# Kernel optimization log

Hardware: AMD Instinct MI355X
Metric: run time of the kernel (lower is better)

## Reference

```python
import jax, jax.numpy as jnp
import numpy as np

N_EMBD = 1024
HEAD_SIZE = 64

def setup_inputs() -> dict:
    key = jax.random.key(0)
    kx, kk, kq, kv = jax.random.split(key, 4)
    x = jax.random.normal(kx, (8, 2048, N_EMBD), dtype=jnp.float32)
    scale = 1.0 / np.sqrt(N_EMBD)
    # nn.Linear weights are [out, in]; kaiming-uniform-ish init
    Wk = jax.random.uniform(kk, (HEAD_SIZE, N_EMBD), dtype=jnp.float32, minval=-scale, maxval=scale)
    Wq = jax.random.uniform(kq, (HEAD_SIZE, N_EMBD), dtype=jnp.float32, minval=-scale, maxval=scale)
    Wv = jax.random.uniform(kv, (HEAD_SIZE, N_EMBD), dtype=jnp.float32, minval=-scale, maxval=scale)
    return {"x": x, "Wk": Wk, "Wq": Wq, "Wv": Wv}

def reference(x, Wk, Wq, Wv):
    # x: [B, T, E]; W*: [H, E] (torch Linear layout)
    k = jnp.einsum('bte,he->bth', x, Wk)
    q = jnp.einsum('bte,he->bth', x, Wq)
    v = jnp.einsum('bte,he->bth', x, Wv)
    inv_sqrt_h = 1.0 / np.sqrt(HEAD_SIZE)
    wei = jnp.einsum('bth,bsh->bts', q, k) * inv_sqrt_h  # [B, T, T]
    wei = jax.nn.softmax(wei, axis=-1)
    out = jnp.einsum('bts,bsh->bth', wei, v)  # [B, T, H]
    return out
```

## Files before the change

### kernel.cpp

```cpp
#include <hip/hip_runtime.h>
#include <cstdint>

#define NB 8
#define TS 2048
#define NE 1024
#define HD 64
#define MTOT (NB*TS)

typedef float     f4  __attribute__((ext_vector_type(4)));
typedef short     s8v __attribute__((ext_vector_type(8)));
typedef short     s4v __attribute__((ext_vector_type(4)));
typedef int       i4v __attribute__((ext_vector_type(4)));
typedef _Float16  h8  __attribute__((ext_vector_type(8)));

__device__ __forceinline__ short f2bf(float f) {
  union { float f; uint32_t u; } x; x.f = f;
  return (short)((x.u + 0x7FFFu + ((x.u >> 16) & 1u)) >> 16);
}

__device__ __forceinline__ int pack2(float lo, float hi) {
  union { float f; uint32_t u; } a, b; a.f = lo; b.f = hi;
  return (int)__builtin_amdgcn_perm(b.u + 0x8000u, a.u + 0x8000u, 0x07060302u);
}

__device__ __forceinline__ void gl2lds(const void* gptr, void* lptr) {
  auto g = (const __attribute__((address_space(1))) uint32_t*)gptr;
  auto l = (__attribute__((address_space(3))) uint32_t*)lptr;
  __builtin_amdgcn_global_load_lds(g, l, 16, 0, 0);
}

template <int N>
__device__ __forceinline__ void wait_barrier() {
  asm volatile("s_waitcnt vmcnt(%0) lgkmcnt(0)" :: "n"(N) : "memory");
  __builtin_amdgcn_s_barrier();
}

__global__ __launch_bounds__(256) void wconv_kernel(
    const float* __restrict__ Wk, const float* __restrict__ Wq, const float* __restrict__ Wv,
    short* __restrict__ wb)
{
  const int idx = (blockIdx.x * 256 + threadIdx.x) * 4;
  const int p = idx >> 16;
  const int off = idx & 65535;
  const float* W = (p == 0) ? Wq : (p == 1) ? Wk : Wv;
  const float s = (p == 0) ? 0.18033688011112042f : 1.0f;
  const float4 v = *(const float4*)&W[off];
  s4v h; h[0] = f2bf(v.x*s); h[1] = f2bf(v.y*s); h[2] = f2bf(v.z*s); h[3] = f2bf(v.w*s);
  *(s4v*)&wb[idx] = h;
}

__global__ __launch_bounds__(256) void proj_kernel(
    const float* __restrict__ x, const short* __restrict__ wb,
    short* __restrict__ qo, short* __restrict__ ko, _Float16* __restrict__ vo)
{
  __shared__ float Xs[4][32][64];
  __shared__ short Ws[2][192][64];
  const int tid = threadIdx.x;
  const int wv = tid >> 6, lane = tid & 63, n = lane & 15, quad = lane >> 4;
  const int mg = wv & 1, cg = wv >> 1;
  const int r0 = blockIdx.x * 32;
  const int xrow = lane >> 4, xslot = lane & 15;
  const int wrow = lane >> 3, wslot = lane & 7;

  auto dmaX = [&](int c, int buf) {
#pragma unroll
    for (int u = 0; u < 2; ++u) {
      const int R0 = (wv * 2 + u) * 4;
      const int row = R0 + xrow;
      const int gs = (xslot + row) & 15;
      gl2lds(&x[(size_t)(r0 + row) * NE + c * 64 + gs * 4], &Xs[buf][R0][0]);
    }
  };
  auto dmaW = [&](int c, int buf) {
#pragma unroll
    for (int u = 0; u < 6; ++u) {
      const int C0 = (wv * 6 + u) * 8;
      const int col = C0 + wrow;
      const int gs = (wslot + col) & 7;
      gl2lds(&wb[(size_t)col * NE + c * 64 + gs * 8], &Ws[buf][C0][0]);
    }
  };

  const f4 fz = {0.f, 0.f, 0.f, 0.f};
  f4 acc[6] = {fz, fz, fz, fz, fz, fz};

  auto compute = [&](int bw, int bx) {
    s8v a[2];
    const int row = mg * 16 + n;
#pragma unroll
    for (int kc = 0; kc < 2; ++kc) {
      const int u0 = kc * 8 + quad * 2;
      const float* pr = &Xs[bx][row][0];
      const f4 f0 = *(const f4*)(pr + (((u0    ) - row) & 15) * 4);
      const f4 f1 = *(const f4*)(pr + (((u0 + 1) - row) & 15) * 4);
      i4v ai;
      ai[0] = pack2(f0[0], f0[1]); ai[1] = pack2(f0[2], f0[3]);
      ai[2] = pack2(f1[0], f1[1]); ai[3] = pack2(f1[2], f1[3]);
      a[kc] = __builtin_bit_cast(s8v, ai);
    }
#pragma unroll
    for (int nf = 0; nf < 6; ++nf) {
      const int col = cg * 96 + nf * 16 + n;
      const s8v b0 = *(const s8v*)&Ws[bw][col][(((0 + quad) - col) & 7) * 8];
      const s8v b1 = *(const s8v*)&Ws[bw][col][(((4 + quad) - col) & 7) * 8];
      acc[nf] = __builtin_amdgcn_mfma_f32_16x16x32_bf16(a[0], b0, acc[nf], 0, 0, 0);
      acc[nf] = __builtin_amdgcn_mfma_f32_16x16x32_bf16(a[1], b1, acc[nf], 0, 0, 0);
    }
  };

  dmaW(0, 0); dmaX(0, 0); dmaX(1, 1); dmaX(2, 2);
  wait_barrier<4>();

  for (int t = 0; t < 16; ++t) {
    if (t <= 14) dmaW(t + 1, (t + 1) & 1);
    if (t <= 12) dmaX(t + 3, (t + 3) & 3);
    compute(t & 1, t & 3);
    if (t <= 12)      wait_barrier<2>();
    else if (t <= 14) wait_barrier<0>();
  }

#pragma unroll
  for (int nf = 0; nf < 6; ++nf) {
    const int gc = cg * 96 + nf * 16;
    const int p = gc >> 6;
    const int rcol = (gc & 63) + n;
#pragma unroll
    for (int i = 0; i < 4; ++i) {
      const int R = r0 + mg * 16 + quad * 4 + i;
      const float av = acc[nf][i];
      if (p == 0)      qo[(size_t)R * HD + rcol] = f2bf(av);
      else if (p == 1) ko[(size_t)R * HD + rcol] = f2bf(av);
      else {
        const int t2 = R & (TS - 1), b = t2 & 31;
        const int pos = (t2 & ~31) | (((b >> 2) & 3) << 3) | (((b >> 4) & 1) << 2) | (b & 3);
        vo[(size_t)(R >> 11) * HD * TS + (size_t)rcol * TS + pos] = (_Float16)av;
      }
    }
  }
}

__global__ __launch_bounds__(512) void attn_kernel(
    const short* __restrict__ q, const short* __restrict__ k,
    const _Float16* __restrict__ vT, float* __restrict__ out)
{
  __shared__ __align__(16) char smem[98304];
  const int tid = threadIdx.x;
  const int wv = tid >> 6, lane = tid & 63, n = lane & 15, quad = lane >> 4;
  const int kq = wv & 3, qg = wv >> 2;
  const int batch = blockIdx.x & 7;
  const int qgb = blockIdx.x >> 3;
  const int m0 = batch * TS + qgb * 64;
  const short*    kb = k  + (size_t)batch * TS * HD;
  const _Float16* vb = vT + (size_t)batch * HD * TS;
  const int drow = lane >> 3, dslot = lane & 7;
  const f4 fz = {0.f, 0.f, 0.f, 0.f};

  auto kbuf = [&](int buf) { return (short*)(smem + (kq * 3 + buf) * 8192); };

  auto dmaK = [&](int tt, int buf) {
    const int c = kq * 8 + tt;
#pragma unroll
    for (int u = 0; u < 4; ++u) {
      const int K0 = (qg * 4 + u) * 8;
      const int key = K0 + drow;
      const int gs = (dslot + key) & 7;
      gl2lds(&kb[(size_t)(c * 64 + key) * HD + gs * 8], kbuf(buf) + K0 * 64);
    }
  };

  s8v qf[2][2];
#pragma unroll
  for (int qh = 0; qh < 2; ++qh)
#pragma unroll
    for (int kc = 0; kc < 2; ++kc)
      qf[qh][kc] = *(const s8v*)&q[(size_t)(m0 + qg * 32 + qh * 16 + n) * HD + kc * 32 + quad * 8];

  f4 o[2][4] = {{fz, fz, fz, fz}, {fz, fz, fz, fz}};
  f4 lD[2] = {fz, fz};
  h8 ones;
#pragma unroll
  for (int j = 0; j < 8; ++j) ones[j] = (_Float16)1.0f;

  dmaK(0, 0); dmaK(1, 1);
  wait_barrier<4>();

  for (int t = 0; t < 8; ++t) {
    const int buf = t % 3;
    const int c = kq * 8 + t;

    h8 vfr[2][4];
#pragma unroll
    for (int pr = 0; pr < 2; ++pr)
#pragma unroll
      for (int g = 0; g < 4; ++g)
        vfr[pr][g] = *(const h8*)&vb[(size_t)(g * 16 + n) * TS + c * 64 + (pr * 4 + quad) * 8];

    if (t <= 5) dmaK(t + 2, (t + 2) % 3);

    const short* ks = kbuf(buf);
    s8v kf[4][2];
#pragma unroll
    for (int f = 0; f < 4; ++f)
#pragma unroll
      for (int kc = 0; kc < 2; ++kc) {
        const int key = f * 16 + n;
        kf[f][kc] = *(const s8v*)&ks[key * 64 + (((kc * 4 + quad) - key) & 7) * 8];
      }

    f4 st[2][4];
#pragma unroll
    for (int qh = 0; qh < 2; ++qh)
#pragma unroll
      for (int f = 0; f < 4; ++f) {
        st[qh][f] = __builtin_amdgcn_mfma_f32_16x16x32_bf16(kf[f][0], qf[qh][0], fz, 0, 0, 0);
        st[qh][f] = __builtin_amdgcn_mfma_f32_16x16x32_bf16(kf[f][1], qf[qh][1], st[qh][f], 0, 0, 0);
      }

    h8 pa[2][2];
#pragma unroll
    for (int qh = 0; qh < 2; ++qh)
#pragma unroll
      for (int pr = 0; pr < 2; ++pr)
#pragma unroll
        for (int hf = 0; hf < 2; ++hf)
#pragma unroll
          for (int i = 0; i < 4; ++i)
            pa[qh][pr][hf * 4 + i] = (_Float16)__builtin_amdgcn_exp2f(st[qh][pr * 2 + hf][i]);

#pragma unroll
    for (int pr = 0; pr < 2; ++pr) {
#pragma unroll
      for (int qh = 0; qh < 2; ++qh)
        lD[qh] = __builtin_amdgcn_mfma_f32_16x16x32_f16(pa[qh][pr], ones, lD[qh], 0, 0, 0);
#pragma unroll
      for (int g = 0; g < 4; ++g)
#pragma unroll
        for (int qh = 0; qh < 2; ++qh)
          o[qh][g] = __builtin_amdgcn_mfma_f32_16x16x32_f16(pa[qh][pr], vfr[pr][g], o[qh][g], 0, 0, 0);
    }

    if (t <= 5)      wait_barrier<4>();
    else if (t == 6) wait_barrier<0>();
  }

  __syncthreads();

  float* o_c = (float*)smem;
  float* l_c = (float*)(smem + 69632);
  if (n == 0)
#pragma unroll
    for (int qh = 0; qh < 2; ++qh)
#pragma unroll
      for (int i = 0; i < 4; ++i)
        l_c[kq * 64 + qg * 32 + qh * 16 + quad * 4 + i] = lD[qh][i];
#pragma unroll
  for (int qh = 0; qh < 2; ++qh)
#pragma unroll
    for (int g = 0; g < 4; ++g)
#pragma unroll
      for (int i = 0; i < 4; ++i)
        o_c[kq * 4352 + (qg * 32 + qh * 16 + quad * 4 + i) * 68 + g * 16 + n] = o[qh][g][i];
  __syncthreads();

#pragma unroll
  for (int rep = 0; rep < 2; ++rep) {
    const int idx = tid + rep * 512;
    const int qr = idx >> 4, d4 = (idx & 15) * 4;
    float L = 0.f;
    f4 r = fz;
#pragma unroll
    for (int c2 = 0; c2 < 4; ++c2) {
      L += l_c[c2 * 64 + qr];
      r += *(const f4*)&o_c[c2 * 4352 + qr * 68 + d4];
    }
    const float inv = 1.0f / L;
    r[0] *= inv; r[1] *= inv; r[2] *= inv; r[3] *= inv;
    *(f4*)&out[(size_t)(m0 + qr) * HD + d4] = r;
  }
}

extern "C" void kernel_launch(void* const* d_in, const int* in_sizes, int n_in,
                              void* d_out, int out_size, void* d_ws, size_t ws_size,
                              hipStream_t stream) {
  const float* x  = (const float*)d_in[0];
  const float* Wk = (const float*)d_in[1];
  const float* Wq = (const float*)d_in[2];
  const float* Wv = (const float*)d_in[3];
  float* out = (float*)d_out;

  short* qb = (short*)d_ws;
  short* kb = qb + (size_t)MTOT * HD;
  _Float16* vb = (_Float16*)(kb + (size_t)MTOT * HD);
  short* wb = (short*)(vb + (size_t)NB * HD * TS);

  wconv_kernel<<<192, 256, 0, stream>>>(Wk, Wq, Wv, wb);
  proj_kernel<<<MTOT / 32, 256, 0, stream>>>(x, wb, qb, kb, vb);
  attn_kernel<<<MTOT / 64, 512, 0, stream>>>(qb, kb, vb, out);
}
```

Baseline: 139.7 us.

## Stage V tiles through LDS with async DMA alongside K, double-buffered

V fragments are no longer loaded straight from global memory into registers. They are now DMA'd into LDS with the same swizzled global_load_lds path as K. The K ring goes from three buffers to two, and V gets a matching double buffer, growing shared memory to 128KB. An extra LDS-done barrier comes before each refill so a buffer is not overwritten while still being read. This trades extra barriers and larger LDS use for coalesced, asynchronous V loads and fewer scattered direct reads.

```diff
diff --git a/kernel.cpp b/kernel.cpp
--- a/kernel.cpp
+++ b/kernel.cpp
@@ -32,6 +32,11 @@
 template <int N>
 __device__ __forceinline__ void wait_barrier() {
   asm volatile("s_waitcnt vmcnt(%0) lgkmcnt(0)" :: "n"(N) : "memory");
+  __builtin_amdgcn_s_barrier();
+}
+
+__device__ __forceinline__ void lds_done_barrier() {
+  asm volatile("s_waitcnt lgkmcnt(0)" ::: "memory");
   __builtin_amdgcn_s_barrier();
 }
 
@@ -143,7 +148,7 @@
     const short* __restrict__ q, const short* __restrict__ k,
     const _Float16* __restrict__ vT, float* __restrict__ out)
 {
-  __shared__ __align__(16) char smem[98304];
+  __shared__ __align__(16) char smem[131072];
   const int tid = threadIdx.x;
   const int wv = tid >> 6, lane = tid & 63, n = lane & 15, quad = lane >> 4;
   const int kq = wv & 3, qg = wv >> 2;
@@ -155,9 +160,10 @@
   const int drow = lane >> 3, dslot = lane & 7;
   const f4 fz = {0.f, 0.f, 0.f, 0.f};
 
-  auto kbuf = [&](int buf) { return (short*)(smem + (kq * 3 + buf) * 8192); };
-
-  auto dmaK = [&](int tt, int buf) {
+  auto kbuf = [&](int buf) { return (short*)   (smem +         (kq * 2 + buf) * 8192); };
+  auto vbuf = [&](int buf) { return (_Float16*)(smem + 65536 + (kq * 2 + buf) * 8192); };
+
+  auto dmaKV = [&](int tt, int buf) {
     const int c = kq * 8 + tt;
 #pragma unroll
     for (int u = 0; u < 4; ++u) {
@@ -166,6 +172,13 @@
       const int gs = (dslot + key) & 7;
       gl2lds(&kb[(size_t)(c * 64 + key) * HD + gs * 8], kbuf(buf) + K0 * 64);
     }
+#pragma unroll
+    for (int u = 0; u < 4; ++u) {
+      const int D0 = (qg * 4 + u) * 8;
+      const int d = D0 + drow;
+      const int gs = (dslot + d) & 7;
+      gl2lds(&vb[(size_t)d * TS + c * 64 + gs * 8], vbuf(buf) + D0 * 64);
+    }
   };
 
   s8v qf[2][2];
@@ -181,40 +194,26 @@
 #pragma unroll
   for (int j = 0; j < 8; ++j) ones[j] = (_Float16)1.0f;
 
-  dmaK(0, 0); dmaK(1, 1);
-  wait_barrier<4>();
+  dmaKV(0, 0); dmaKV(1, 1);
+  wait_barrier<8>();
 
   for (int t = 0; t < 8; ++t) {
-    const int buf = t % 3;
-    const int c = kq * 8 + t;
-
-    h8 vfr[2][4];
-#pragma unroll
-    for (int pr = 0; pr < 2; ++pr)
-#pragma unroll
-      for (int g = 0; g < 4; ++g)
-        vfr[pr][g] = *(const h8*)&vb[(size_t)(g * 16 + n) * TS + c * 64 + (pr * 4 + quad) * 8];
-
-    if (t <= 5) dmaK(t + 2, (t + 2) % 3);
-
-    const short* ks = kbuf(buf);
-    s8v kf[4][2];
-#pragma unroll
-    for (int f = 0; f < 4; ++f)
-#pragma unroll
-      for (int kc = 0; kc < 2; ++kc) {
-        const int key = f * 16 + n;
-        kf[f][kc] = *(const s8v*)&ks[key * 64 + (((kc * 4 + quad) - key) & 7) * 8];
+    const int buf = t & 1;
+    const short*    ks = kbuf(buf);
+    const _Float16* vs = vbuf(buf);
+
+    f4 st[2][4];
+#pragma unroll
+    for (int f = 0; f < 4; ++f) {
+      const int key = f * 16 + n;
+      const s8v k0 = *(const s8v*)&ks[key * 64 + (((0 + quad) - key) & 7) * 8];
+      const s8v k1 = *(const s8v*)&ks[key * 64 + (((4 + quad) - key) & 7) * 8];
+#pragma unroll
+      for (int qh = 0; qh < 2; ++qh) {
+        st[qh][f] = __builtin_amdgcn_mfma_f32_16x16x32_bf16(k0, qf[qh][0], fz, 0, 0, 0);
+        st[qh][f] = __builtin_amdgcn_mfma_f32_16x16x32_bf16(k1, qf[qh][1], st[qh][f], 0, 0, 0);
       }
-
-    f4 st[2][4];
-#pragma unroll
-    for (int qh = 0; qh < 2; ++qh)
-#pragma unroll
-      for (int f = 0; f < 4; ++f) {
-        st[qh][f] = __builtin_amdgcn_mfma_f32_16x16x32_bf16(kf[f][0], qf[qh][0], fz, 0, 0, 0);
-        st[qh][f] = __builtin_amdgcn_mfma_f32_16x16x32_bf16(kf[f][1], qf[qh][1], st[qh][f], 0, 0, 0);
-      }
+    }
 
     h8 pa[2][2];
 #pragma unroll
@@ -233,14 +232,22 @@
       for (int qh = 0; qh < 2; ++qh)
         lD[qh] = __builtin_amdgcn_mfma_f32_16x16x32_f16(pa[qh][pr], ones, lD[qh], 0, 0, 0);
 #pragma unroll
-      for (int g = 0; g < 4; ++g)
+      for (int g = 0; g < 4; ++g) {
+        const int d = g * 16 + n;
+        const h8 vf = *(const h8*)&vs[d * 64 + (((pr * 4 + quad) - d) & 7) * 8];
 #pragma unroll
         for (int qh = 0; qh < 2; ++qh)
-          o[qh][g] = __builtin_amdgcn_mfma_f32_16x16x32_f16(pa[qh][pr], vfr[pr][g], o[qh][g], 0, 0, 0);
-    }
-
-    if (t <= 5)      wait_barrier<4>();
-    else if (t == 6) wait_barrier<0>();
+          o[qh][g] = __builtin_amdgcn_mfma_f32_16x16x32_f16(pa[qh][pr], vf, o[qh][g], 0, 0, 0);
+      }
+    }
+
+    if (t <= 5) {
+      lds_done_barrier();
+      dmaKV(t + 2, buf);
+      wait_barrier<8>();
+    } else if (t == 6) {
+      wait_barrier<0>();
+    }
   }
 
   __syncthreads();
```

After: 128.9 us. 1.08x faster.
